# Kernel optimization log

Hardware: AMD Instinct MI355X
Metric: run time of the kernel (lower is better)

Reference implementation:

```python
import jax, jax.numpy as jnp
import numpy as np
from jax import lax

HEADS = 8
LN_EPS = 1e-5


def setup_inputs() -> dict:
    key = jax.random.key(0)
    k = jax.random.split(key, 8)
    B, C, H, W, r = 4, 64, 64, 64, 4
    T = H * W
    x = jax.random.normal(k[0], (B, C, H, W), dtype=jnp.float32)
    conv_w = jax.random.normal(k[1], (C, C, r, r), dtype=jnp.float32) * 0.02  # OIHW
    conv_b = jnp.zeros((C,), dtype=jnp.float32)
    ln_g = jnp.ones((C,), dtype=jnp.float32)
    ln_b = jnp.zeros((C,), dtype=jnp.float32)
    Wqkv = jax.random.normal(k[2], (C, 3 * C), dtype=jnp.float32) * 0.02  # to_qvk (no bias)
    W0 = jax.random.normal(k[3], (C, C), dtype=jnp.float32) * 0.02  # output proj (no bias)
    E = jax.random.normal(k[4], (T, T // 4), dtype=jnp.float32)  # Linformer proj (randn in torch fwd)
    return {"x": x, "conv_w": conv_w, "conv_b": conv_b, "ln_g": ln_g,
            "ln_b": ln_b, "Wqkv": Wqkv, "W0": W0, "E": E}


def _layernorm2d(y, g, b):
    # LayerNorm over channel dim of NCHW (torch: permute to NHWC, LN last dim)
    yt = y.transpose(0, 2, 3, 1)  # b h w c
    mu = yt.mean(-1, keepdims=True)
    var = ((yt - mu) ** 2).mean(-1, keepdims=True)
    yt = (yt - mu) * lax.rsqrt(var + LN_EPS) * g + b
    return yt.transpose(0, 3, 1, 2)


def reference(x, conv_w, conv_b, ln_g, ln_b, Wqkv, W0, E):
    B, C, H, W = x.shape
    T = H * W
    dh = C // HEADS
    r = conv_w.shape[-1]

    # reducer: conv(stride=r) + LayerNorm2d. NOTE: faithful to the torch module,
    # this result is computed but NEVER used by the output (dead code in source).
    red = lax.conv_general_dilated(x, conv_w, (r, r), 'VALID',
                                   dimension_numbers=('NCHW', 'OIHW', 'NCHW'))
    red = red + conv_b[None, :, None, None]
    _red = _layernorm2d(red, ln_g, ln_b)  # unused, matches source

    # tokens from full-resolution x: b c h w -> b (h w) c
    xf = x.reshape(B, C, T).transpose(0, 2, 1)  # [B,T,C]
    qkv = xf @ Wqkv  # [B,T,3C]
    # rearrange 'b t (d k h)' with k=3, h=HEADS -> composite order (d, k, h)
    qkv = qkv.reshape(B, T, dh, 3, HEADS)
    q = qkv[:, :, :, 0, :].transpose(0, 3, 1, 2)  # [B,h,T,d]
    kk = qkv[:, :, :, 1, :].transpose(0, 3, 1, 2)
    v = qkv[:, :, :, 2, :].transpose(0, 3, 1, 2)

    # Linformer low-rank projection of V and K: [B,h,T,d] x [T,k] -> [B,h,k,d]
    v = jnp.einsum('bhjd,jk->bhkd', v, E)
    kk = jnp.einsum('bhjd,jk->bhkd', kk, E)

    scale = dh ** -0.5
    scores = jnp.einsum('bhid,bhjd->bhij', q, kk) * scale  # [B,h,T,k]
    attn = jax.nn.softmax(scores, axis=-1)
    out = jnp.einsum('bhij,bhjd->bhid', attn, v)  # [B,h,T,d]

    out = out.transpose(0, 2, 1, 3).reshape(B, T, C)  # b h i d -> b i (h d)
    out = out @ W0  # [B,T,C]
    return out.transpose(0, 2, 1).reshape(B, C, H, W)
```

## Files before the change

### kernel.cpp

```cpp
#include <hip/hip_runtime.h>

#define T_DIM 4096
#define KD    1024
#define SCALE2 (0.35355339059327373f * 1.4426950408889634f)
#define VT_PITCH 1032
#define XS_PITCH 264
#define XP_PITCH 17
#define WK_PITCH 136

extern "C" __device__ float __ocml_native_exp2_f32(float);

typedef __attribute__((ext_vector_type(8))) short bf16x8;
typedef __attribute__((ext_vector_type(4))) float f32x4;
typedef __attribute__((ext_vector_type(16))) float f32x16;

__device__ inline unsigned short f2bf(float f) {
  unsigned u = __float_as_uint(f);
  unsigned r = u + 0x7fffu + ((u >> 16) & 1u);
  return (unsigned short)(r >> 16);
}

__device__ inline unsigned cvt_pk_bf16(float a, float b) {
  unsigned ua = __float_as_uint(a); ua += 0x7fffu + ((ua >> 16) & 1u);
  unsigned ub = __float_as_uint(b); ub += 0x7fffu + ((ub >> 16) & 1u);
  return (ua >> 16) | (ub & 0xffff0000u);
}

__device__ inline bf16x8 mk8(unsigned a, unsigned b, unsigned c, unsigned d) {
  union { unsigned u[4]; bf16x8 v; } x;
  x.u[0] = a; x.u[1] = b; x.u[2] = c; x.u[3] = d; return x.v;
}

__global__ __launch_bounds__(512) void k_front(const float* __restrict__ x,
                                               const float* __restrict__ E,
                                               const float* __restrict__ Wqkv,
                                               uint2* __restrict__ Kg,
                                               unsigned short* __restrict__ Vg,
                                               float* __restrict__ Q,
                                               float* __restrict__ out) {
  __shared__ __attribute__((aligned(16))) float SMEM[8 * 64 * XP_PITCH];
  __shared__ __attribute__((aligned(16))) float Wkvs[64 * WK_PITCH];
  unsigned short* xs = (unsigned short*)SMEM;
  float* XPs = SMEM;

  const int bid = blockIdx.x;
  const int tid = threadIdx.x;

  if (bid < 256) {
    const int kb = bid >> 2;
    const int b  = bid & 3;
    const int k0 = kb * 16;
    const int lane = tid & 63, w = tid >> 6;
    const int li = lane & 15, lg = lane >> 4;

#pragma unroll
    for (int i = 0; i < 16; ++i) {
      const int idx = tid + i * 512;
      const int c = idx >> 7, j = idx & 127;
      const int cg = j >> 3, d = j & 7;
      const int sel = (cg < 8) ? 1 : 2, h = cg & 7;
      Wkvs[c * WK_PITCH + j] = Wqkv[c * 192 + sel * 8 + h + d * 24];
    }

    f32x4 acc[4] = {};
    const int tl  = (tid & 127) * 2;
    const int chp = tid >> 7;
    const int tloc = w * 32 + lg * 8;

    for (int ct = 0; ct < 16; ++ct) {
      const float* xb = x + ((size_t)b * 64 + chp) * T_DIM + ct * 256 + tl;
#pragma unroll 4
      for (int it = 0; it < 16; ++it) {
        const int c = it * 4 + chp;
        float2 v = *(const float2*)(xb + (size_t)(it * 4) * T_DIM);
        *(unsigned*)(&xs[c * XS_PITCH + tl]) = cvt_pk_bf16(v.x, v.y);
      }
      __syncthreads();

      const int tb = ct * 256 + tloc;
      float bv[8];
#pragma unroll
      for (int j = 0; j < 8; ++j)
        bv[j] = E[(size_t)(tb + j) * KD + k0 + li];
      bf16x8 bq = mk8(cvt_pk_bf16(bv[0], bv[1]), cvt_pk_bf16(bv[2], bv[3]),
                      cvt_pk_bf16(bv[4], bv[5]), cvt_pk_bf16(bv[6], bv[7]));
#pragma unroll
      for (int mt = 0; mt < 4; ++mt) {
        bf16x8 af8 = *(const bf16x8*)(&xs[(mt * 16 + li) * XS_PITCH + tloc]);
        acc[mt] = __builtin_amdgcn_mfma_f32_16x16x32_bf16(af8, bq, acc[mt], 0, 0, 0);
      }
      __syncthreads();
    }

#pragma unroll
    for (int mt = 0; mt < 4; ++mt)
#pragma unroll
      for (int r = 0; r < 4; ++r)
        XPs[(w * 64 + mt * 16 + lg * 4 + r) * XP_PITCH + li] = acc[mt][r];
    __syncthreads();

#pragma unroll
    for (int i = 0; i < 2; ++i) {
      const int idx = tid + i * 512;
      const int c = idx >> 4, k = idx & 15;
      float s = 0.f;
#pragma unroll
      for (int wp = 0; wp < 8; ++wp) s += XPs[(wp * 64 + c) * XP_PITCH + k];
      XPs[c * XP_PITCH + k] = s;
    }
    __syncthreads();

    {
      const int k  = tid & 15;
      const int cg = (tid >> 4) & 15;
      const int dh = tid >> 8;
      float a4[4] = {0.f, 0.f, 0.f, 0.f};
#pragma unroll 8
      for (int c = 0; c < 64; ++c) {
        const float xv = XPs[c * XP_PITCH + k];
        const float4 wv = *(const float4*)(&Wkvs[c * WK_PITCH + cg * 8 + dh * 4]);
        a4[0] += xv * wv.x; a4[1] += xv * wv.y;
        a4[2] += xv * wv.z; a4[3] += xv * wv.w;
      }
      const int h = cg & 7, bh = b * 8 + h, kk2 = k0 + k;
      if (cg < 8) {
        Kg[(size_t)bh * 2048 + kk2 * 2 + dh] =
            make_uint2(cvt_pk_bf16(a4[0] * SCALE2, a4[1] * SCALE2),
                       cvt_pk_bf16(a4[2] * SCALE2, a4[3] * SCALE2));
      } else {
#pragma unroll
        for (int d = 0; d < 4; ++d)
          Vg[(size_t)(bh * 8 + dh * 4 + d) * KD + kk2] = f2bf(a4[d]);
      }
    }
  } else {
    const int idx = bid - 256;
    const int g  = idx & 7;
    const int tt = (idx >> 3) & 7;
    const int b  = idx >> 6;
    const int t  = tt * 512 + tid;
    const int col0 = g * 24;

    {
      float4* o4 = (float4*)out;
      o4[(size_t)idx * 1024 + tid]       = make_float4(0.f, 0.f, 0.f, 0.f);
      o4[(size_t)idx * 1024 + tid + 512] = make_float4(0.f, 0.f, 0.f, 0.f);
    }

    float acc[8];
#pragma unroll
    for (int j = 0; j < 8; ++j) acc[j] = 0.f;
    const float* xb = x + (size_t)b * 64 * T_DIM + t;
#pragma unroll 4
    for (int c = 0; c < 64; ++c) {
      float xv = xb[(size_t)c * T_DIM];
      const float* wr = Wqkv + c * 192 + col0;
#pragma unroll
      for (int h = 0; h < 8; ++h) acc[h] += xv * wr[h];
    }
#pragma unroll
    for (int h = 0; h < 8; ++h)
      Q[(((size_t)(b * 8 + h)) * 8 + g) * T_DIM + t] = acc[h];
  }
}

__global__ __launch_bounds__(256, 4) void k_attn(const float* __restrict__ Q,
                                              const uint2* __restrict__ Kg,
                                              const unsigned short* __restrict__ Vg,
                                              const float* __restrict__ W0,
                                              float* __restrict__ out) {
  __shared__ __attribute__((aligned(16))) unsigned short Kt[1024 * 8];
  __shared__ unsigned short Vt[9 * VT_PITCH];
  __shared__ float W0s[512];
  const int bh = blockIdx.x;
  const int tid = threadIdx.x;
  const int b = bh >> 3, h = bh & 7;

  const uint4* kg4 = (const uint4*)(Kg + (size_t)bh * 2048);
  uint4* kt4 = (uint4*)Kt;
#pragma unroll
  for (int it = 0; it < 4; ++it)
    kt4[it * 256 + tid] = kg4[it * 256 + tid];
  const unsigned* vg = (const unsigned*)(Vg + (size_t)bh * 8192);
#pragma unroll
  for (int dd = 0; dd < 8; ++dd) {
#pragma unroll
    for (int it = 0; it < 2; ++it) {
      const int j2 = it * 256 + tid;
      *(unsigned*)(Vt + dd * VT_PITCH + j2 * 2) = vg[dd * 512 + j2];
    }
  }
#pragma unroll
  for (int it = 0; it < 2; ++it)
    *(unsigned*)(Vt + 8 * VT_PITCH + (it * 256 + tid) * 2) = 0x3F803F80u;
  W0s[tid]       = W0[h * 512 + tid];
  W0s[tid + 256] = W0[h * 512 + tid + 256];
  __syncthreads();

  const int lane = tid & 63, w = tid >> 6;
  const int icol = lane & 31, half = lane >> 5;
  const int i0w = blockIdx.y * 128 + w * 32;

  bf16x8 qf8 = {};
  if (lane < 32) {
    const float* qp = Q + (size_t)bh * 8 * T_DIM + i0w + icol;
    float q0 = qp[0],          q1 = qp[T_DIM],     q2 = qp[2 * T_DIM];
    float q3 = qp[3 * T_DIM],  q4 = qp[4 * T_DIM], q5 = qp[5 * T_DIM];
    float q6 = qp[6 * T_DIM],  q7 = qp[7 * T_DIM];
    qf8 = mk8(cvt_pk_bf16(q0, q1), cvt_pk_bf16(q2, q3),
              cvt_pk_bf16(q4, q5), cvt_pk_bf16(q6, q7));
  }

  f32x16 accO = {};
  for (int jt = 0; jt < 1024; jt += 32) {
    bf16x8 kf8 = {};
    if (lane < 32) kf8 = *(const bf16x8*)(&Kt[(jt + lane) * 8]);
    f32x16 z = {};
    __builtin_amdgcn_s_setprio(1);
    f32x16 st = __builtin_amdgcn_mfma_f32_32x32x16_bf16(kf8, qf8, z, 0, 0, 0);
    __builtin_amdgcn_s_setprio(0);

    unsigned e0, e1, e2, e3, e4, e5, e6, e7;
    {
      float p0  = __ocml_native_exp2_f32(st[0]),  p1  = __ocml_native_exp2_f32(st[1]);
      float p2  = __ocml_native_exp2_f32(st[2]),  p3  = __ocml_native_exp2_f32(st[3]);
      float p4  = __ocml_native_exp2_f32(st[4]),  p5  = __ocml_native_exp2_f32(st[5]);
      float p6  = __ocml_native_exp2_f32(st[6]),  p7  = __ocml_native_exp2_f32(st[7]);
      float p8  = __ocml_native_exp2_f32(st[8]),  p9  = __ocml_native_exp2_f32(st[9]);
      float p10 = __ocml_native_exp2_f32(st[10]), p11 = __ocml_native_exp2_f32(st[11]);
      float p12 = __ocml_native_exp2_f32(st[12]), p13 = __ocml_native_exp2_f32(st[13]);
      float p14 = __ocml_native_exp2_f32(st[14]), p15 = __ocml_native_exp2_f32(st[15]);
      asm("v_cvt_pk_bf16_f32 %0, %1, %2" : "=v"(e0) : "v"(p0),  "v"(p1));
      asm("v_cvt_pk_bf16_f32 %0, %1, %2" : "=v"(e1) : "v"(p2),  "v"(p3));
      asm("v_cvt_pk_bf16_f32 %0, %1, %2" : "=v"(e2) : "v"(p4),  "v"(p5));
      asm("v_cvt_pk_bf16_f32 %0, %1, %2" : "=v"(e3) : "v"(p6),  "v"(p7));
      asm("v_cvt_pk_bf16_f32 %0, %1, %2" : "=v"(e4) : "v"(p8),  "v"(p9));
      asm("v_cvt_pk_bf16_f32 %0, %1, %2" : "=v"(e5) : "v"(p10), "v"(p11));
      asm("v_cvt_pk_bf16_f32 %0, %1, %2" : "=v"(e6) : "v"(p12), "v"(p13));
      asm("v_cvt_pk_bf16_f32 %0, %1, %2" : "=v"(e7) : "v"(p14), "v"(p15));
    }
    asm("v_permlane32_swap_b32 %0, %1" : "+v"(e0), "+v"(e2));
    asm("v_permlane32_swap_b32 %0, %1" : "+v"(e1), "+v"(e3));
    asm("v_permlane32_swap_b32 %0, %1" : "+v"(e4), "+v"(e6));
    asm("v_permlane32_swap_b32 %0, %1" : "+v"(e5), "+v"(e7));

    bf16x8 va0 = {}, va1 = {};
    if (icol < 9) {
      const unsigned short* vp = Vt + icol * VT_PITCH + jt + half * 8;
      va0 = *(const bf16x8*)(vp);
      va1 = *(const bf16x8*)(vp + 16);
    }
    __builtin_amdgcn_s_setprio(1);
    accO = __builtin_amdgcn_mfma_f32_32x32x16_bf16(va0, mk8(e0, e1, e2, e3), accO, 0, 0, 0);
    accO = __builtin_amdgcn_mfma_f32_32x32x16_bf16(va1, mk8(e4, e5, e6, e7), accO, 0, 0, 0);
    __builtin_amdgcn_s_setprio(0);
  }

  __syncthreads();
  float* OwW = (float*)Kt + w * 256;

  {
    float inv = 1.0f / __shfl(accO[4], icol);
    float4 o = make_float4(accO[0] * inv, accO[1] * inv,
                           accO[2] * inv, accO[3] * inv);
    *(float4*)(OwW + icol * 8 + half * 4) = o;
  }

  const int tok = icol, ch = half;
  float ov[8];
#pragma unroll
  for (int d = 0; d < 8; ++d) ov[d] = OwW[tok * 8 + d];
#pragma unroll 4
  for (int j = 0; j < 32; ++j) {
    const int c = ch * 32 + j;
    float a = 0.f;
#pragma unroll
    for (int d = 0; d < 8; ++d) a += ov[d] * W0s[d * 64 + c];
    atomicAdd(out + ((size_t)b * 64 + c) * T_DIM + i0w + tok, a);
  }
}

extern "C" void kernel_launch(void* const* d_in, const int* in_sizes, int n_in,
                              void* d_out, int out_size, void* d_ws, size_t ws_size,
                              hipStream_t stream) {
  const float* x    = (const float*)d_in[0];
  const float* Wqkv = (const float*)d_in[5];
  const float* W0   = (const float*)d_in[6];
  const float* E    = (const float*)d_in[7];
  float* out = (float*)d_out;

  float* Q           = (float*)d_ws;
  uint2* Kg          = (uint2*)(Q + 1048576);
  unsigned short* Vg = (unsigned short*)(Kg + 65536);

  k_front <<<dim3(512),    512, 0, stream>>>(x, E, Wqkv, Kg, Vg, Q, out);
  k_attn  <<<dim3(32, 32), 256, 0, stream>>>(Q, Kg, Vg, W0, out);
}
```

Before: 156.6 us.

## Process all heads per block in attention with streamed K/V and direct output projection

The attention kernel now assigns each 512-thread block all 8 heads of a 32-token tile, one wavefront per head. K/V chunks are streamed through double-buffered LDS instead of loading each head's full K/V up front. With every head in the block, the W0 output projection is done in-block and written directly, which removes the zero-fill of the output in the front kernel and the per-head atomicAdd traffic. It also remaps the front kernel's block-to-(kb,b) assignment. The cost is more K/V reloading across blocks (each block streams all 8 heads' K/V) and a barrier per chunk.

New measurement: 139.8 us. 1.12x faster.

```diff
diff --git a/kernel.cpp b/kernel.cpp
--- a/kernel.cpp
+++ b/kernel.cpp
@@ -3,10 +3,10 @@
 #define T_DIM 4096
 #define KD    1024
 #define SCALE2 (0.35355339059327373f * 1.4426950408889634f)
-#define VT_PITCH 1032
 #define XS_PITCH 264
 #define XP_PITCH 17
 #define WK_PITCH 136
+#define VC_H 648
 
 extern "C" __device__ float __ocml_native_exp2_f32(float);
 
@@ -36,8 +36,7 @@
                                                const float* __restrict__ Wqkv,
                                                uint2* __restrict__ Kg,
                                                unsigned short* __restrict__ Vg,
-                                               float* __restrict__ Q,
-                                               float* __restrict__ out) {
+                                               float* __restrict__ Q) {
   __shared__ __attribute__((aligned(16))) float SMEM[8 * 64 * XP_PITCH];
   __shared__ __attribute__((aligned(16))) float Wkvs[64 * WK_PITCH];
   unsigned short* xs = (unsigned short*)SMEM;
@@ -47,8 +46,8 @@
   const int tid = threadIdx.x;
 
   if (bid < 256) {
-    const int kb = bid >> 2;
-    const int b  = bid & 3;
+    const int kb = (bid & 7) + 8 * (bid >> 5);
+    const int b  = (bid >> 3) & 3;
     const int k0 = kb * 16;
     const int lane = tid & 63, w = tid >> 6;
     const int li = lane & 15, lg = lane >> 4;
@@ -141,12 +140,6 @@
     const int t  = tt * 512 + tid;
     const int col0 = g * 24;
 
-    {
-      float4* o4 = (float4*)out;
-      o4[(size_t)idx * 1024 + tid]       = make_float4(0.f, 0.f, 0.f, 0.f);
-      o4[(size_t)idx * 1024 + tid + 512] = make_float4(0.f, 0.f, 0.f, 0.f);
-    }
-
     float acc[8];
 #pragma unroll
     for (int j = 0; j < 8; ++j) acc[j] = 0.f;
@@ -164,46 +157,35 @@
   }
 }
 
-__global__ __launch_bounds__(256, 4) void k_attn(const float* __restrict__ Q,
-                                              const uint2* __restrict__ Kg,
-                                              const unsigned short* __restrict__ Vg,
-                                              const float* __restrict__ W0,
-                                              float* __restrict__ out) {
-  __shared__ __attribute__((aligned(16))) unsigned short Kt[1024 * 8];
-  __shared__ unsigned short Vt[9 * VT_PITCH];
-  __shared__ float W0s[512];
-  const int bh = blockIdx.x;
+__global__ __launch_bounds__(512, 4) void k_attn(const float* __restrict__ Q,
+                                                 const uint2* __restrict__ Kg,
+                                                 const unsigned short* __restrict__ Vg,
+                                                 const float* __restrict__ W0,
+                                                 float* __restrict__ out) {
+  __shared__ __attribute__((aligned(16))) unsigned short Kc[2][8 * 64 * 8];
+  __shared__ __attribute__((aligned(16))) unsigned short Vc[2][8 * VC_H];
+  __shared__ __attribute__((aligned(16))) float W0s[64 * 64];
+
+  const int iy = blockIdx.x;
+  const int b  = blockIdx.y;
   const int tid = threadIdx.x;
-  const int b = bh >> 3, h = bh & 7;
-
-  const uint4* kg4 = (const uint4*)(Kg + (size_t)bh * 2048);
-  uint4* kt4 = (uint4*)Kt;
-#pragma unroll
-  for (int it = 0; it < 4; ++it)
-    kt4[it * 256 + tid] = kg4[it * 256 + tid];
-  const unsigned* vg = (const unsigned*)(Vg + (size_t)bh * 8192);
-#pragma unroll
-  for (int dd = 0; dd < 8; ++dd) {
-#pragma unroll
-    for (int it = 0; it < 2; ++it) {
-      const int j2 = it * 256 + tid;
-      *(unsigned*)(Vt + dd * VT_PITCH + j2 * 2) = vg[dd * 512 + j2];
-    }
-  }
-#pragma unroll
-  for (int it = 0; it < 2; ++it)
-    *(unsigned*)(Vt + 8 * VT_PITCH + (it * 256 + tid) * 2) = 0x3F803F80u;
-  W0s[tid]       = W0[h * 512 + tid];
-  W0s[tid + 256] = W0[h * 512 + tid + 256];
-  __syncthreads();
-
-  const int lane = tid & 63, w = tid >> 6;
+  const int w = tid >> 6;
+  const int lane = tid & 63;
   const int icol = lane & 31, half = lane >> 5;
-  const int i0w = blockIdx.y * 128 + w * 32;
+  const int i0 = iy * 32;
+  const int bh = b * 8 + w;
+
+#pragma unroll
+  for (int i = 0; i < 8; ++i) W0s[tid + i * 512] = W0[tid + i * 512];
+
+  {
+    const int bu = tid >> 8, h = (tid >> 5) & 7, j2 = tid & 31;
+    *(unsigned*)(&Vc[bu][h * VC_H + 8 * 72 + j2 * 2]) = 0x3F803F80u;
+  }
 
   bf16x8 qf8 = {};
   if (lane < 32) {
-    const float* qp = Q + (size_t)bh * 8 * T_DIM + i0w + icol;
+    const float* qp = Q + (size_t)bh * 8 * T_DIM + i0 + icol;
     float q0 = qp[0],          q1 = qp[T_DIM],     q2 = qp[2 * T_DIM];
     float q3 = qp[3 * T_DIM],  q4 = qp[4 * T_DIM], q5 = qp[5 * T_DIM];
     float q6 = qp[6 * T_DIM],  q7 = qp[7 * T_DIM];
@@ -211,72 +193,121 @@
               cvt_pk_bf16(q4, q5), cvt_pk_bf16(q6, q7));
   }
 
+  const uint4* kg4    = (const uint4*)Kg + (size_t)b * 8192;
+  const unsigned* vg2 = (const unsigned*)Vg + (size_t)b * 32768;
+
+  {
+    const int h = tid >> 6, j = tid & 63;
+    *(uint4*)(&Kc[0][(h * 64 + j) * 8]) = kg4[h * 1024 + j];
+#pragma unroll
+    for (int i = 0; i < 4; ++i) {
+      const int idx = tid + i * 512;
+      const int hh = idx >> 8, d = (idx >> 5) & 7, j2 = idx & 31;
+      *(unsigned*)(&Vc[0][hh * VC_H + d * 72 + j2 * 2]) = vg2[(hh * 8 + d) * 512 + j2];
+    }
+  }
+  __syncthreads();
+
   f32x16 accO = {};
-  for (int jt = 0; jt < 1024; jt += 32) {
-    bf16x8 kf8 = {};
-    if (lane < 32) kf8 = *(const bf16x8*)(&Kt[(jt + lane) * 8]);
-    f32x16 z = {};
-    __builtin_amdgcn_s_setprio(1);
-    f32x16 st = __builtin_amdgcn_mfma_f32_32x32x16_bf16(kf8, qf8, z, 0, 0, 0);
-    __builtin_amdgcn_s_setprio(0);
-
-    unsigned e0, e1, e2, e3, e4, e5, e6, e7;
-    {
-      float p0  = __ocml_native_exp2_f32(st[0]),  p1  = __ocml_native_exp2_f32(st[1]);
-      float p2  = __ocml_native_exp2_f32(st[2]),  p3  = __ocml_native_exp2_f32(st[3]);
-      float p4  = __ocml_native_exp2_f32(st[4]),  p5  = __ocml_native_exp2_f32(st[5]);
-      float p6  = __ocml_native_exp2_f32(st[6]),  p7  = __ocml_native_exp2_f32(st[7]);
-      float p8  = __ocml_native_exp2_f32(st[8]),  p9  = __ocml_native_exp2_f32(st[9]);
-      float p10 = __ocml_native_exp2_f32(st[10]), p11 = __ocml_native_exp2_f32(st[11]);
-      float p12 = __ocml_native_exp2_f32(st[12]), p13 = __ocml_native_exp2_f32(st[13]);
-      float p14 = __ocml_native_exp2_f32(st[14]), p15 = __ocml_native_exp2_f32(st[15]);
-      asm("v_cvt_pk_bf16_f32 %0, %1, %2" : "=v"(e0) : "v"(p0),  "v"(p1));
-      asm("v_cvt_pk_bf16_f32 %0, %1, %2" : "=v"(e1) : "v"(p2),  "v"(p3));
-      asm("v_cvt_pk_bf16_f32 %0, %1, %2" : "=v"(e2) : "v"(p4),  "v"(p5));
-      asm("v_cvt_pk_bf16_f32 %0, %1, %2" : "=v"(e3) : "v"(p6),  "v"(p7));
-      asm("v_cvt_pk_bf16_f32 %0, %1, %2" : "=v"(e4) : "v"(p8),  "v"(p9));
-      asm("v_cvt_pk_bf16_f32 %0, %1, %2" : "=v"(e5) : "v"(p10), "v"(p11));
-      asm("v_cvt_pk_bf16_f32 %0, %1, %2" : "=v"(e6) : "v"(p12), "v"(p13));
-      asm("v_cvt_pk_bf16_f32 %0, %1, %2" : "=v"(e7) : "v"(p14), "v"(p15));
-    }
-    asm("v_permlane32_swap_b32 %0, %1" : "+v"(e0), "+v"(e2));
-    asm("v_permlane32_swap_b32 %0, %1" : "+v"(e1), "+v"(e3));
-    asm("v_permlane32_swap_b32 %0, %1" : "+v"(e4), "+v"(e6));
-    asm("v_permlane32_swap_b32 %0, %1" : "+v"(e5), "+v"(e7));
-
-    bf16x8 va0 = {}, va1 = {};
-    if (icol < 9) {
-      const unsigned short* vp = Vt + icol * VT_PITCH + jt + half * 8;
-      va0 = *(const bf16x8*)(vp);
-      va1 = *(const bf16x8*)(vp + 16);
-    }
-    __builtin_amdgcn_s_setprio(1);
-    accO = __builtin_amdgcn_mfma_f32_32x32x16_bf16(va0, mk8(e0, e1, e2, e3), accO, 0, 0, 0);
-    accO = __builtin_amdgcn_mfma_f32_32x32x16_bf16(va1, mk8(e4, e5, e6, e7), accO, 0, 0, 0);
-    __builtin_amdgcn_s_setprio(0);
-  }
-
-  __syncthreads();
-  float* OwW = (float*)Kt + w * 256;
-
+  int buf = 0;
+  for (int jc = 0; jc < 16; ++jc) {
+    uint4 kreg = {}; unsigned vreg[4] = {};
+    if (jc < 15) {
+      const int h = tid >> 6, j = tid & 63;
+      kreg = kg4[h * 1024 + (jc + 1) * 64 + j];
+#pragma unroll
+      for (int i = 0; i < 4; ++i) {
+        const int idx = tid + i * 512;
+        const int hh = idx >> 8, d = (idx >> 5) & 7, j2 = idx & 31;
+        vreg[i] = vg2[(hh * 8 + d) * 512 + (jc + 1) * 32 + j2];
+      }
+    }
+
+#pragma unroll
+    for (int sub = 0; sub < 2; ++sub) {
+      const int jl = sub * 32;
+      bf16x8 kf8 = {};
+      if (lane < 32) kf8 = *(const bf16x8*)(&Kc[buf][(w * 64 + jl + lane) * 8]);
+      f32x16 z = {};
+      __builtin_amdgcn_s_setprio(1);
+      f32x16 st = __builtin_amdgcn_mfma_f32_32x32x16_bf16(kf8, qf8, z, 0, 0, 0);
+      __builtin_amdgcn_s_setprio(0);
+
+      unsigned e0, e1, e2, e3, e4, e5, e6, e7;
+      {
+        float p0  = __ocml_native_exp2_f32(st[0]),  p1  = __ocml_native_exp2_f32(st[1]);
+        float p2  = __ocml_native_exp2_f32(st[2]),  p3  = __ocml_native_exp2_f32(st[3]);
+        float p4  = __ocml_native_exp2_f32(st[4]),  p5  = __ocml_native_exp2_f32(st[5]);
+        float p6  = __ocml_native_exp2_f32(st[6]),  p7  = __ocml_native_exp2_f32(st[7]);
+        float p8  = __ocml_native_exp2_f32(st[8]),  p9  = __ocml_native_exp2_f32(st[9]);
+        float p10 = __ocml_native_exp2_f32(st[10]), p11 = __ocml_native_exp2_f32(st[11]);
+        float p12 = __ocml_native_exp2_f32(st[12]), p13 = __ocml_native_exp2_f32(st[13]);
+        float p14 = __ocml_native_exp2_f32(st[14]), p15 = __ocml_native_exp2_f32(st[15]);
+        asm("v_cvt_pk_bf16_f32 %0, %1, %2" : "=v"(e0) : "v"(p0),  "v"(p1));
+        asm("v_cvt_pk_bf16_f32 %0, %1, %2" : "=v"(e1) : "v"(p2),  "v"(p3));
+        asm("v_cvt_pk_bf16_f32 %0, %1, %2" : "=v"(e2) : "v"(p4),  "v"(p5));
+        asm("v_cvt_pk_bf16_f32 %0, %1, %2" : "=v"(e3) : "v"(p6),  "v"(p7));
+        asm("v_cvt_pk_bf16_f32 %0, %1, %2" : "=v"(e4) : "v"(p8),  "v"(p9));
+        asm("v_cvt_pk_bf16_f32 %0, %1, %2" : "=v"(e5) : "v"(p10), "v"(p11));
+        asm("v_cvt_pk_bf16_f32 %0, %1, %2" : "=v"(e6) : "v"(p12), "v"(p13));
+        asm("v_cvt_pk_bf16_f32 %0, %1, %2" : "=v"(e7) : "v"(p14), "v"(p15));
+      }
+      asm("v_permlane32_swap_b32 %0, %1" : "+v"(e0), "+v"(e2));
+      asm("v_permlane32_swap_b32 %0, %1" : "+v"(e1), "+v"(e3));
+      asm("v_permlane32_swap_b32 %0, %1" : "+v"(e4), "+v"(e6));
+      asm("v_permlane32_swap_b32 %0, %1" : "+v"(e5), "+v"(e7));
+
+      bf16x8 va0 = {}, va1 = {};
+      if (icol < 9) {
+        const unsigned short* vp = &Vc[buf][w * VC_H + icol * 72 + jl + half * 8];
+        va0 = *(const bf16x8*)(vp);
+        va1 = *(const bf16x8*)(vp + 16);
+      }
+      __builtin_amdgcn_s_setprio(1);
+      accO = __builtin_amdgcn_mfma_f32_32x32x16_bf16(va0, mk8(e0, e1, e2, e3), accO, 0, 0, 0);
+      accO = __builtin_amdgcn_mfma_f32_32x32x16_bf16(va1, mk8(e4, e5, e6, e7), accO, 0, 0, 0);
+      __builtin_amdgcn_s_setprio(0);
+    }
+
+    if (jc < 15) {
+      const int h = tid >> 6, j = tid & 63;
+      *(uint4*)(&Kc[buf ^ 1][(h * 64 + j) * 8]) = kreg;
+#pragma unroll
+      for (int i = 0; i < 4; ++i) {
+        const int idx = tid + i * 512;
+        const int hh = idx >> 8, d = (idx >> 5) & 7, j2 = idx & 31;
+        *(unsigned*)(&Vc[buf ^ 1][hh * VC_H + d * 72 + j2 * 2]) = vreg[i];
+      }
+    }
+    __syncthreads();
+    buf ^= 1;
+  }
+
+  float* Os = (float*)Kc;
   {
     float inv = 1.0f / __shfl(accO[4], icol);
-    float4 o = make_float4(accO[0] * inv, accO[1] * inv,
-                           accO[2] * inv, accO[3] * inv);
-    *(float4*)(OwW + icol * 8 + half * 4) = o;
-  }
-
-  const int tok = icol, ch = half;
-  float ov[8];
-#pragma unroll
-  for (int d = 0; d < 8; ++d) ov[d] = OwW[tok * 8 + d];
-#pragma unroll 4
-  for (int j = 0; j < 32; ++j) {
-    const int c = ch * 32 + j;
-    float a = 0.f;
-#pragma unroll
-    for (int d = 0; d < 8; ++d) a += ov[d] * W0s[d * 64 + c];
-    atomicAdd(out + ((size_t)b * 64 + c) * T_DIM + i0w + tok, a);
+    if (lane < 32 || half) {
+      float4 o = make_float4(accO[0] * inv, accO[1] * inv,
+                             accO[2] * inv, accO[3] * inv);
+      *(float2*)(&Os[icol * 66 + w * 8 + half * 4])     = make_float2(o.x, o.y);
+      *(float2*)(&Os[icol * 66 + w * 8 + half * 4 + 2]) = make_float2(o.z, o.w);
+    }
+  }
+  __syncthreads();
+
+  {
+    const int tok = tid & 31, cq = tid >> 5;
+    float o4[4] = {0.f, 0.f, 0.f, 0.f};
+#pragma unroll 8
+    for (int hd = 0; hd < 64; ++hd) {
+      const float ov = Os[tok * 66 + hd];
+      const float4 wv = *(const float4*)(&W0s[hd * 64 + cq * 4]);
+      o4[0] += ov * wv.x; o4[1] += ov * wv.y;
+      o4[2] += ov * wv.z; o4[3] += ov * wv.w;
+    }
+#pragma unroll
+    for (int cc = 0; cc < 4; ++cc)
+      out[((size_t)b * 64 + cq * 4 + cc) * T_DIM + i0 + tok] = o4[cc];
   }
 }
 
@@ -293,6 +324,6 @@
   uint2* Kg          = (uint2*)(Q + 1048576);
   unsigned short* Vg = (unsigned short*)(Kg + 65536);
 
-  k_front <<<dim3(512),    512, 0, stream>>>(x, E, Wqkv, Kg, Vg, Q, out);
-  k_attn  <<<dim3(32, 32), 256, 0, stream>>>(Q, Kg, Vg, W0, out);
-}
+  k_front <<<dim3(512),    512, 0, stream>>>(x, E, Wqkv, Kg, Vg, Q);
+  k_attn  <<<dim3(128, 4), 512, 0, stream>>>(Q, Kg, Vg, W0, out);
+}
```
